# Optimization experiments

Hardware: AMD Instinct MI355X
Metric: run time of the kernel (lower is better)

The kernel has to match this reference:

```python
import jax, jax.numpy as jnp
import numpy as np
from jax import lax

B, V, K, E = 32768, 256, 4, 2048
INTERVENTION_STRENGTH = 1.0
PROP_SCALE = 0.1
N_ROUNDS = 3


def setup_inputs() -> dict:
    key = jax.random.key(0)
    ks = jax.random.split(key, 20)
    s = 0.02
    return {
        "original_data": jax.random.normal(ks[0], (B, V), jnp.float32),
        "intervention_values": jax.random.normal(ks[1], (B, K), jnp.float32),
        "strengths": jax.random.uniform(ks[2], (E,), jnp.float32),
        "intervention_variables": jnp.arange(K, dtype=jnp.int32),
        "cause_idx": jax.random.randint(ks[3], (E,), 0, V, jnp.int32),
        "effect_idx": jax.random.randint(ks[4], (E,), 0, V, jnp.int32),
        # per-intervention-variable estimator MLPs: Linear(V,64) -> ReLU -> Linear(64,V)
        "est_W1": jax.random.normal(ks[5], (K, 64, V), jnp.float32) * s,
        "est_b1": jnp.zeros((K, 64), jnp.float32),
        "est_W2": jax.random.normal(ks[6], (K, V, 64), jnp.float32) * s,
        "est_b2": jnp.zeros((K, V), jnp.float32),
        # plausibility scorer: Linear(3V,128) -> ReLU -> Linear(128,64) -> ReLU -> Linear(64,1) -> Sigmoid
        "pl_W1": jax.random.normal(ks[7], (128, 3 * V), jnp.float32) * s,
        "pl_b1": jnp.zeros((128,), jnp.float32),
        "pl_W2": jax.random.normal(ks[8], (64, 128), jnp.float32) * s,
        "pl_b2": jnp.zeros((64,), jnp.float32),
        "pl_W3": jax.random.normal(ks[9], (1, 64), jnp.float32) * s,
        "pl_b3": jnp.zeros((1,), jnp.float32),
    }


def _propagate(data, cause_idx, effect_idx, strengths):
    # Faithful sequential in-place edge updates (effect of edge k may feed edge k+1).
    def step(d, ces):
        c, e, st = ces
        infl = d[:, c] * (st * PROP_SCALE)  # [B]
        return d.at[:, e].add(infl), None

    def round_body(d, _):
        d, _ = lax.scan(step, d, (cause_idx, effect_idx, strengths))
        return d, None

    d, _ = lax.scan(round_body, data, None, length=N_ROUNDS)
    return d


def reference(original_data, intervention_values, strengths,
              est_W1, est_b1, est_W2, est_b2,
              pl_W1, pl_b1, pl_W2, pl_b2, pl_W3, pl_b3,
              intervention_variables, cause_idx, effect_idx):
    x = original_data  # [B, V]
    ivars = intervention_variables  # [K] int, constant

    # do-intervention: overwrite selected columns
    intervened = x.at[:, ivars].set(intervention_values)  # [B, V]

    # intervention effect estimators, vectorized over the K intervened variables
    h = jax.nn.relu(jnp.einsum('bv,kov->bko', x, est_W1) + est_b1)          # [B, K, 64]
    eff = jnp.einsum('bko,kvo->bkv', h, est_W2) + est_b2                     # [B, K, V]
    mag = jnp.abs(intervention_values - x[:, ivars])                         # [B, K]
    intervention_effects = jnp.einsum('bkv,bk->bv', eff, mag) * INTERVENTION_STRENGTH  # [B, V]

    # sequential causal propagation over edge list, 3 rounds
    final_cf = _propagate(intervened + intervention_effects, cause_idx, effect_idx, strengths)

    # plausibility scorer MLP
    pin = jnp.concatenate([x, intervened, final_cf], axis=1)                 # [B, 3V]
    p = jax.nn.relu(pin @ pl_W1.T + pl_b1)
    p = jax.nn.relu(p @ pl_W2.T + pl_b2)
    plaus = jax.nn.sigmoid(p @ pl_W3.T + pl_b3)                              # [B, 1]

    impact = jnp.linalg.norm(final_cf - x, axis=1, keepdims=True)            # [B, 1]
    return final_cf, intervention_effects, plaus, impact
```

## Files before the change

kernel.cpp:

```cpp
#include <hip/hip_runtime.h>

#define BDIM 32768
#define VDIM 256
#define KVAR 4
#define EDIM 2048
#define SEGS 16
#define SEGLEN 128

typedef __attribute__((ext_vector_type(8))) short short8;
typedef __attribute__((ext_vector_type(4))) float f32x4;

__device__ __forceinline__ unsigned short f2b(float f){
  union { float f; unsigned u; } v; v.f = f;
  unsigned r = v.u + 0x7FFFu + ((v.u >> 16) & 1u);
  return (unsigned short)(r >> 16);
}
__device__ __forceinline__ float b2f(unsigned short h){
  union { unsigned u; float f; } v; v.u = ((unsigned)h) << 16;
  return v.f;
}
__device__ __forceinline__ short8 ldb8(const unsigned short* p){
  return *(const short8*)p;
}

__device__ __forceinline__ void gl_lds16(const unsigned short* g, unsigned short* l){
  __builtin_amdgcn_global_load_lds(
      (const __attribute__((address_space(1))) unsigned int*)g,
      (__attribute__((address_space(3))) unsigned int*)l, 16, 0, 0);
}

__device__ __forceinline__ void stage256(const unsigned short* Bt, int kB,
                                         int w, int lane, unsigned short* Bs){
#pragma unroll
  for (int i = 0; i < 4; i++){
    int g8 = i*8 + w;
    int r  = g8*8 + (lane >> 3);
    int s  = lane & 7;
    gl_lds16(Bt + (size_t)r*VDIM + kB + ((s ^ (r & 7)) << 3),
             Bs + (size_t)g8*512);
  }
}
__device__ __forceinline__ void stage128(const unsigned short* Bt, int kB,
                                         int w, int lane, unsigned short* Bs){
#pragma unroll
  for (int i = 0; i < 2; i++){
    int g8 = i*8 + w;
    int r  = g8*8 + (lane >> 3);
    int s  = lane & 7;
    gl_lds16(Bt + (size_t)r*VDIM + kB + ((s ^ (r & 7)) << 3),
             Bs + (size_t)g8*512);
  }
}
__device__ __forceinline__ void stage64xb(const unsigned short* XBg, int rowBlk, int kB,
                                          int w, int lane, unsigned short* xbs){
  int r = w*8 + (lane >> 3);
  int s = lane & 7;
  gl_lds16(XBg + (size_t)(rowBlk + r)*VDIM + kB + ((s ^ (r & 7)) << 3),
           xbs + (size_t)w*512);
}

__device__ __forceinline__ short8 bs_frag(const unsigned short* Bs, int c, int klocal){
  int slot = klocal >> 3;
  return *(const short8*)&Bs[(size_t)c*64 + ((slot ^ (c & 7)) << 3)];
}

template<int NF>
__device__ __forceinline__ void mm_xA(const unsigned short* xbs, const unsigned short* Bs,
                                      int rl0, int c0, int kb, f32x4 (&acc)[2][NF])
{
  int sw = (rl0 & 7) << 3;
#pragma unroll
  for (int k = 0; k < 2; k++){
    int kl = k*32 + kb;
    short8 a0 = *(const short8*)&xbs[(size_t)rl0*64 + (kl ^ sw)];
    short8 a1 = *(const short8*)&xbs[(size_t)(rl0+16)*64 + (kl ^ sw)];
#pragma unroll
    for (int fn = 0; fn < NF; fn++){
      short8 b = bs_frag(Bs, c0 + fn*16, kl);
      acc[0][fn] = __builtin_amdgcn_mfma_f32_16x16x32_bf16(a0, b, acc[0][fn], 0, 0, 0);
      acc[1][fn] = __builtin_amdgcn_mfma_f32_16x16x32_bf16(a1, b, acc[1][fn], 0, 0, 0);
    }
  }
}
template<int NF>
__device__ __forceinline__ void mm_lA(const unsigned short* Alds, int ldaE,
                                      const unsigned short* Bs,
                                      int rl0, int c0, int kb, int kB,
                                      f32x4 (&acc)[2][NF])
{
  int sw = (rl0 & 7) << 3;
#pragma unroll
  for (int k = 0; k < 2; k++){
    int ka = kB + k*32 + kb;
    short8 a0 = *(const short8*)&Alds[(size_t)rl0 * ldaE + (ka ^ sw)];
    short8 a1 = *(const short8*)&Alds[(size_t)(rl0+16) * ldaE + (ka ^ sw)];
#pragma unroll
    for (int fn = 0; fn < NF; fn++){
      short8 b = bs_frag(Bs, c0 + fn*16, k*32 + kb);
      acc[0][fn] = __builtin_amdgcn_mfma_f32_16x16x32_bf16(a0, b, acc[0][fn], 0, 0, 0);
      acc[1][fn] = __builtin_amdgcn_mfma_f32_16x16x32_bf16(a1, b, acc[1][fn], 0, 0, 0);
    }
  }
}
template<int NF, int KSZ>
__device__ __forceinline__ void mm_l1(const unsigned short* Alds, int ldaE,
                                      const unsigned short* Bt, int ldb,
                                      int rl0, int c0, int kb,
                                      f32x4 (&acc)[NF])
{
  int sw = (rl0 & 7) << 3;
#pragma unroll
  for (int k0 = 0; k0 < KSZ; k0 += 32){
    int ka = k0 + kb;
    short8 a0 = *(const short8*)&Alds[(size_t)rl0 * ldaE + (ka ^ sw)];
#pragma unroll
    for (int fn = 0; fn < NF; fn++){
      short8 b = ldb8(Bt + (size_t)(c0 + fn*16)*ldb + ka);
      acc[fn] = __builtin_amdgcn_mfma_f32_16x16x32_bf16(a0, b, acc[fn], 0, 0, 0);
    }
  }
}

__global__ __launch_bounds__(256) void prep_seg(
    const float* X, const float* IV, const int* ivars,
    const float* eW1, const float* eW2, const float* pW1, const float* pW2,
    const int* cidx, const int* eidx, const float* stren,
    unsigned short* XB,
    unsigned short* bt1, unsigned short* bt2,
    unsigned short* w1ab, unsigned short* w1c,
    unsigned short* w2bf, float* w1bcol, int* colmap,
    float* delta, float* segs)
{
  if (blockIdx.x < 1024){
    __shared__ int lc[SEGLEN];
    __shared__ int le[SEGLEN];
    __shared__ float la[SEGLEN];
    int bid = blockIdx.x;
    int seg = bid >> 6;
    int rowbase = (bid & 63) * 4;
    int w = threadIdx.x >> 6, lane = threadIdx.x & 63;
    int row = rowbase + w;
    int k0 = seg * SEGLEN;
    for (int t = threadIdx.x; t < SEGLEN; t += 256){
      lc[t] = cidx[k0 + t]; le[t] = eidx[k0 + t]; la[t] = stren[k0 + t] * 0.1f;
    }
    __syncthreads();
    float r0 = (row == lane)        ? 1.f : 0.f;
    float r1 = (row == lane + 64)   ? 1.f : 0.f;
    float r2 = (row == lane + 128)  ? 1.f : 0.f;
    float r3 = (row == lane + 192)  ? 1.f : 0.f;
    for (int t = 0; t < SEGLEN; t++){
      int cs = __builtin_amdgcn_readfirstlane(lc[t]);
      int es = __builtin_amdgcn_readfirstlane(le[t]);
      float a = la[t];
      float vr;
      switch (cs >> 6){ case 0: vr = r0; break; case 1: vr = r1; break;
                        case 2: vr = r2; break; default: vr = r3; }
      float v = __shfl(vr, cs & 63, 64);
      float add = (lane == (es & 63)) ? a * v : 0.f;
      switch (es >> 6){ case 0: r0 += add; break; case 1: r1 += add; break;
                        case 2: r2 += add; break; default: r3 += add; }
    }
    float* out = segs + (size_t)seg * 65536 + (size_t)row * 256;
    out[lane] = r0; out[lane + 64] = r1; out[lane + 128] = r2; out[lane + 192] = r3;
    return;
  }
  int stride = 1024 * 256;
  int g0 = (blockIdx.x - 1024) * 256 + threadIdx.x;
  for (int i = g0; i < (BDIM * VDIM) / 8; i += stride){
    const float* p = X + (size_t)i * 8;
    f32x4 lo = *(const f32x4*)p;
    f32x4 hi = *(const f32x4*)(p + 4);
    short8 r;
    r[0]=(short)f2b(lo[0]); r[1]=(short)f2b(lo[1]); r[2]=(short)f2b(lo[2]); r[3]=(short)f2b(lo[3]);
    r[4]=(short)f2b(hi[0]); r[5]=(short)f2b(hi[1]); r[6]=(short)f2b(hi[2]); r[7]=(short)f2b(hi[3]);
    *(short8*)(XB + (size_t)i * 8) = r;
  }
  for (int i = g0; i < 65536; i += stride) bt1[i] = f2b(eW1[i]);
  for (int i = g0; i < 65536; i += stride){
    int v = i >> 8, r = i & 255;
    bt2[i] = f2b(eW2[(r >> 6) * 16384 + v * 64 + (r & 63)]);
  }
  for (int i = g0; i < 32768; i += stride){
    int o = i >> 8, v = i & 255;
    w1ab[i] = f2b(pW1[o*768 + v] + pW1[o*768 + 256 + v]);
    w1c[i]  = f2b(pW1[o*768 + 512 + v]);
  }
  for (int i = g0; i < 8192; i += stride) w2bf[i] = f2b(pW2[i]);
  for (int i = g0; i < 512; i += stride){
    int o = i >> 2, k = i & 3;
    w1bcol[i] = pW1[o*768 + 256 + ivars[k]];
  }
  for (int i = g0; i < VDIM; i += stride){
    int m = -1;
#pragma unroll
    for (int k = 0; k < KVAR; k++) if (ivars[k] == i) m = k;
    colmap[i] = m;
  }
  for (int i = g0; i < BDIM * KVAR; i += stride){
    int b = i >> 2, k = i & 3;
    delta[i] = IV[i] - X[(size_t)b * VDIM + ivars[k]];
  }
}

__global__ __launch_bounds__(256) void combine4(const float* S, float* Out)
{
  int m = blockIdx.x >> 6;
  int rb = (blockIdx.x & 63) * 4;
  int c = threadIdx.x;
  __shared__ float v[4][256];
  const float* base = S + (size_t)m * 4 * 65536;
#pragma unroll
  for (int r = 0; r < 4; r++) v[r][c] = base[(size_t)(rb + r) * 256 + c];
  __syncthreads();
  for (int p = 1; p < 4; p++){
    const float* Bm = base + (size_t)p * 65536;
    float a0 = 0.f, a1 = 0.f, a2 = 0.f, a3 = 0.f;
    for (int k = 0; k < 256; k += 4){
      f32x4 v0 = *(const f32x4*)&v[0][k];
      f32x4 v1 = *(const f32x4*)&v[1][k];
      f32x4 v2 = *(const f32x4*)&v[2][k];
      f32x4 v3 = *(const f32x4*)&v[3][k];
#pragma unroll
      for (int j = 0; j < 4; j++){
        float bk = Bm[(size_t)(k + j) * 256 + c];
        a0 += v0[j] * bk; a1 += v1[j] * bk; a2 += v2[j] * bk; a3 += v3[j] * bk;
      }
    }
    __syncthreads();
    v[0][c] = a0; v[1][c] = a1; v[2][c] = a2; v[3][c] = a3;
    __syncthreads();
  }
#pragma unroll
  for (int r = 0; r < 4; r++) Out[(size_t)m * 65536 + (size_t)(rb + r) * 256 + c] = v[r][c];
}

__global__ __launch_bounds__(256) void powM(const float* R, unsigned short* Mt)
{
  int rb = blockIdx.x * 4;
  int c = threadIdx.x;
  __shared__ float v[4][256];
#pragma unroll
  for (int r = 0; r < 4; r++) v[r][c] = R[(size_t)(rb + r) * 256 + c];
  __syncthreads();
  for (int p = 0; p < 2; p++){
    float a0 = 0.f, a1 = 0.f, a2 = 0.f, a3 = 0.f;
    for (int k = 0; k < 256; k += 4){
      f32x4 v0 = *(const f32x4*)&v[0][k];
      f32x4 v1 = *(const f32x4*)&v[1][k];
      f32x4 v2 = *(const f32x4*)&v[2][k];
      f32x4 v3 = *(const f32x4*)&v[3][k];
#pragma unroll
      for (int j = 0; j < 4; j++){
        float bk = R[(size_t)(k + j) * 256 + c];
        a0 += v0[j] * bk; a1 += v1[j] * bk; a2 += v2[j] * bk; a3 += v3[j] * bk;
      }
    }
    __syncthreads();
    v[0][c] = a0; v[1][c] = a1; v[2][c] = a2; v[3][c] = a3;
    __syncthreads();
  }
#pragma unroll
  for (int r = 0; r < 4; r++) Mt[(size_t)c * 256 + (rb + r)] = f2b(v[r][c]);
}

__global__ __launch_bounds__(512, 4) void mega(
    const float* IV, const unsigned short* XB,
    const unsigned short* Bt1, const unsigned short* Bt2, const unsigned short* Mt,
    const unsigned short* W1ab, const unsigned short* W1c, const unsigned short* W2bf,
    const float* eb1, const float* eb2, const float* delta, const int* colmap,
    const float* w1bcol, const float* pb1, const float* pb2,
    const float* W3, const float* pb3,
    float* effOut, float* outF, float* plausOut, float* impOut)
{
  __shared__ unsigned short buf[64 * 256];
  __shared__ unsigned short Bs[256 * 64];
  __shared__ unsigned short xbs[64 * 64];
  __shared__ float impLds[64 * 4];
  int tid = threadIdx.x, w = tid >> 6, lane = tid & 63;
  int rowg = w >> 2, colg = w & 3;
  int rowBlk = blockIdx.x * 64;
  int rl0 = rowg * 32 + (lane & 15);
  int colBase = colg * 64;
  int c0 = colBase + (lane & 15);
  int kb = (lane >> 4) * 8;
  f32x4 acc[2][4];
  unsigned short xcap[2][4][4];

#pragma unroll
  for (int fm = 0; fm < 2; fm++)
#pragma unroll
    for (int fn = 0; fn < 4; fn++) acc[fm][fn] = (f32x4){0.f,0.f,0.f,0.f};
  for (int kc = 0; kc < 4; kc++){
    int kB = kc * 64;
    stage256(Bt1, kB, w, lane, Bs);
    stage64xb(XB, rowBlk, kB, w, lane, xbs);
    __syncthreads();
    __builtin_amdgcn_s_setprio(1);
    mm_xA<4>(xbs, Bs, rl0, c0, kb, acc);
    __builtin_amdgcn_s_setprio(0);
    if (colg == kc){
#pragma unroll
      for (int fm = 0; fm < 2; fm++)
#pragma unroll
        for (int i = 0; i < 4; i++){
          int rl = rowg*32 + fm*16 + (lane >> 4)*4 + i;
          int sw = (rl & 7) << 3;
#pragma unroll
          for (int fn = 0; fn < 4; fn++){
            int lc = fn*16 + (lane & 15);
            xcap[fm][i][fn] = xbs[(size_t)rl*64 + (lc ^ sw)];
          }
        }
    }
    __syncthreads();
  }
  {
    float b1v[4];
#pragma unroll
    for (int fn = 0; fn < 4; fn++) b1v[fn] = eb1[colBase + fn*16 + (lane & 15)];
#pragma unroll
    for (int fm = 0; fm < 2; fm++)
#pragma unroll
      for (int i = 0; i < 4; i++){
        int rl = rowg*32 + fm*16 + (lane >> 4)*4 + i;
        int gr = rowBlk + rl;
        float mg = fabsf(delta[gr*4 + colg]);
        int sw = (rl & 7) << 3;
#pragma unroll
        for (int fn = 0; fn < 4; fn++){
          int col = colBase + fn*16 + (lane & 15);
          float h = acc[fm][fn][i] + b1v[fn];
          h = h > 0.f ? h : 0.f;
          buf[(size_t)rl*256 + (col ^ sw)] = f2b(h * mg);
        }
      }
  }
  __syncthreads();

#pragma unroll
  for (int fm = 0; fm < 2; fm++)
#pragma unroll
    for (int fn = 0; fn < 4; fn++) acc[fm][fn] = (f32x4){0.f,0.f,0.f,0.f};
  for (int kc = 0; kc < 4; kc++){
    int kB = kc * 64;
    stage256(Bt2, kB, w, lane, Bs);
    __syncthreads();
    __builtin_amdgcn_s_setprio(1);
    mm_lA<4>(buf, 256, Bs, rl0, c0, kb, kB, acc);
    __builtin_amdgcn_s_setprio(0);
    __syncthreads();
  }
  {
    float bb0[4], bb1[4], bb2[4], bb3[4];
    int imv[4];
#pragma unroll
    for (int fn = 0; fn < 4; fn++){
      int col = colBase + fn*16 + (lane & 15);
      bb0[fn] = eb2[col]; bb1[fn] = eb2[256 + col];
      bb2[fn] = eb2[512 + col]; bb3[fn] = eb2[768 + col];
      imv[fn] = colmap[col];
    }
#pragma unroll
    for (int fm = 0; fm < 2; fm++)
#pragma unroll
      for (int i = 0; i < 4; i++){
        int rl = rowg*32 + fm*16 + (lane >> 4)*4 + i;
        int gr = rowBlk + rl;
        f32x4 dl = *(const f32x4*)&delta[gr*4];
        float d0a = fabsf(dl[0]), d1a = fabsf(dl[1]), d2a = fabsf(dl[2]), d3a = fabsf(dl[3]);
        int sw = (rl & 7) << 3;
#pragma unroll
        for (int fn = 0; fn < 4; fn++){
          int col = colBase + fn*16 + (lane & 15);
          float eff = acc[fm][fn][i] + d0a*bb0[fn] + d1a*bb1[fn] + d2a*bb2[fn] + d3a*bb3[fn];
          size_t idx = (size_t)gr*VDIM + col;
          effOut[idx] = eff;
          float base = (imv[fn] >= 0) ? IV[gr*4 + imv[fn]] : b2f(xcap[fm][i][fn]);
          buf[(size_t)rl*256 + (col ^ sw)] = f2b(base + eff);
        }
      }
  }
  __syncthreads();

#pragma unroll
  for (int fm = 0; fm < 2; fm++)
#pragma unroll
    for (int fn = 0; fn < 4; fn++) acc[fm][fn] = (f32x4){0.f,0.f,0.f,0.f};
  for (int kc = 0; kc < 4; kc++){
    int kB = kc * 64;
    stage256(Mt, kB, w, lane, Bs);
    __syncthreads();
    __builtin_amdgcn_s_setprio(1);
    mm_lA<4>(buf, 256, Bs, rl0, c0, kb, kB, acc);
    __builtin_amdgcn_s_setprio(0);
    __syncthreads();
  }
  {
#pragma unroll
    for (int fm = 0; fm < 2; fm++)
#pragma unroll
      for (int i = 0; i < 4; i++){
        int rl = rowg*32 + fm*16 + (lane >> 4)*4 + i;
        int gr = rowBlk + rl;
        int sw = (rl & 7) << 3;
        float ss = 0.f;
#pragma unroll
        for (int fn = 0; fn < 4; fn++){
          int col = colBase + fn*16 + (lane & 15);
          size_t idx = (size_t)gr*VDIM + col;
          float fv = acc[fm][fn][i];
          outF[idx] = fv;
          buf[(size_t)rl*256 + (col ^ sw)] = f2b(fv);
          float d = fv - b2f(xcap[fm][i][fn]);
          ss += d * d;
        }
        ss += __shfl_xor(ss, 1, 64); ss += __shfl_xor(ss, 2, 64);
        ss += __shfl_xor(ss, 4, 64); ss += __shfl_xor(ss, 8, 64);
        if ((lane & 15) == 0) impLds[rl*4 + colg] = ss;
      }
  }
  __syncthreads();

  {
    f32x4 a4[2][2];
#pragma unroll
    for (int fm = 0; fm < 2; fm++)
#pragma unroll
      for (int fn = 0; fn < 2; fn++) a4[fm][fn] = (f32x4){0.f,0.f,0.f,0.f};
    int c4 = colg * 32 + (lane & 15);
    for (int kc = 0; kc < 4; kc++){
      int kB = kc * 64;
      stage128(W1ab, kB, w, lane, Bs);
      stage128(W1c,  kB, w, lane, Bs + 8192);
      stage64xb(XB, rowBlk, kB, w, lane, xbs);
      __syncthreads();
      __builtin_amdgcn_s_setprio(1);
      mm_xA<2>(xbs, Bs, rl0, c4, kb, a4);
      mm_lA<2>(buf, 256, Bs + 8192, rl0, c4, kb, kB, a4);
      __builtin_amdgcn_s_setprio(0);
      __syncthreads();
    }
    float bv[2];
    f32x4 wb[2];
#pragma unroll
    for (int fn = 0; fn < 2; fn++){
      int col = colg*32 + fn*16 + (lane & 15);
      bv[fn] = pb1[col];
      wb[fn] = *(const f32x4*)&w1bcol[col*4];
    }
#pragma unroll
    for (int fm = 0; fm < 2; fm++)
#pragma unroll
      for (int i = 0; i < 4; i++){
        int rl = rowg*32 + fm*16 + (lane >> 4)*4 + i;
        int gr = rowBlk + rl;
        f32x4 dl = *(const f32x4*)&delta[gr*4];
        int sw = (rl & 7) << 3;
#pragma unroll
        for (int fn = 0; fn < 2; fn++){
          int col = colg*32 + fn*16 + (lane & 15);
          float p = a4[fm][fn][i] + bv[fn]
                  + dl[0]*wb[fn][0] + dl[1]*wb[fn][1] + dl[2]*wb[fn][2] + dl[3]*wb[fn][3];
          p = p > 0.f ? p : 0.f;
          buf[(size_t)rl*128 + (col ^ sw)] = f2b(p);
        }
      }
  }
  __syncthreads();

  if (w < 4){
    int rl0b = w * 16 + (lane & 15);
    f32x4 a2[4];
#pragma unroll
    for (int fn = 0; fn < 4; fn++) a2[fn] = (f32x4){0.f,0.f,0.f,0.f};
    mm_l1<4, 128>(buf, 128, W2bf, 128, rl0b, (lane & 15), kb, a2);
    float b2v[4], w3v[4];
#pragma unroll
    for (int fn = 0; fn < 4; fn++){
      int col = fn*16 + (lane & 15);
      b2v[fn] = pb2[col]; w3v[fn] = W3[col];
    }
    float b3v = pb3[0];
#pragma unroll
    for (int i = 0; i < 4; i++){
      float s = 0.f;
#pragma unroll
      for (int fn = 0; fn < 4; fn++){
        float p2 = a2[fn][i] + b2v[fn];
        p2 = p2 > 0.f ? p2 : 0.f;
        s += p2 * w3v[fn];
      }
      s += __shfl_xor(s, 1, 64); s += __shfl_xor(s, 2, 64);
      s += __shfl_xor(s, 4, 64); s += __shfl_xor(s, 8, 64);
      if ((lane & 15) == 0){
        int gr = rowBlk + w*16 + (lane >> 4)*4 + i;
        plausOut[gr] = 1.f / (1.f + expf(-(s + b3v)));
      }
    }
  } else if (w == 4){
    f32x4 v = *(const f32x4*)&impLds[lane * 4];
    impOut[rowBlk + lane] = sqrtf(v[0] + v[1] + v[2] + v[3]);
  }
}

#define WS_XB     ((size_t)0)
#define WS_DELTA  ((size_t)16777216)
#define WS_SEG    ((size_t)17301504)
#define WS_T2     ((size_t)21495808)
#define WS_R      ((size_t)22544384)
#define WS_MT     ((size_t)22806528)
#define WS_BT1    ((size_t)22937600)
#define WS_BT2    ((size_t)23068672)
#define WS_W1AB   ((size_t)23199744)
#define WS_W1C    ((size_t)23265280)
#define WS_W2BF   ((size_t)23330816)
#define WS_W1BCOL ((size_t)23347200)
#define WS_COLMAP ((size_t)23349248)

extern "C" void kernel_launch(void* const* d_in, const int* in_sizes, int n_in,
                              void* d_out, int out_size, void* d_ws, size_t ws_size,
                              hipStream_t stream)
{
  const float* X     = (const float*)d_in[0];
  const float* IV    = (const float*)d_in[1];
  const float* STR   = (const float*)d_in[2];
  const int*   IVARS = (const int*)d_in[3];
  const int*   CIDX  = (const int*)d_in[4];
  const int*   EIDX  = (const int*)d_in[5];
  const float* EW1   = (const float*)d_in[6];
  const float* EB1   = (const float*)d_in[7];
  const float* EW2   = (const float*)d_in[8];
  const float* EB2   = (const float*)d_in[9];
  const float* PW1   = (const float*)d_in[10];
  const float* PB1   = (const float*)d_in[11];
  const float* PW2   = (const float*)d_in[12];
  const float* PB2   = (const float*)d_in[13];
  const float* PW3   = (const float*)d_in[14];
  const float* PB3   = (const float*)d_in[15];

  char* ws = (char*)d_ws;
  unsigned short* XB     = (unsigned short*)(ws + WS_XB);
  float*          DELTA  = (float*)(ws + WS_DELTA);
  float*          SEG    = (float*)(ws + WS_SEG);
  float*          T2     = (float*)(ws + WS_T2);
  float*          Rm     = (float*)(ws + WS_R);
  unsigned short* MT     = (unsigned short*)(ws + WS_MT);
  unsigned short* BT1    = (unsigned short*)(ws + WS_BT1);
  unsigned short* BT2    = (unsigned short*)(ws + WS_BT2);
  unsigned short* W1AB   = (unsigned short*)(ws + WS_W1AB);
  unsigned short* W1C    = (unsigned short*)(ws + WS_W1C);
  unsigned short* W2BF   = (unsigned short*)(ws + WS_W2BF);
  float*          W1BCOL = (float*)(ws + WS_W1BCOL);
  int*            COLMAP = (int*)(ws + WS_COLMAP);

  float* outF   = (float*)d_out;
  float* outEff = outF + (size_t)BDIM * VDIM;
  float* outPl  = outEff + (size_t)BDIM * VDIM;
  float* outIm  = outPl + BDIM;

  prep_seg<<<2048, 256, 0, stream>>>(X, IV, IVARS, EW1, EW2, PW1, PW2,
                                     CIDX, EIDX, STR,
                                     XB, BT1, BT2, W1AB, W1C, W2BF, W1BCOL, COLMAP,
                                     DELTA, SEG);
  combine4<<<256, 256, 0, stream>>>(SEG, T2);
  combine4<<<64, 256, 0, stream>>>(T2, Rm);
  powM<<<64, 256, 0, stream>>>(Rm, MT);

  mega<<<512, 512, 0, stream>>>(IV, XB, BT1, BT2, MT, W1AB, W1C, W2BF,
                                EB1, EB2, DELTA, COLMAP, W1BCOL,
                                PB1, PB2, PW3, PB3,
                                outEff, outF, outPl, outIm);

  (void)in_sizes; (void)n_in; (void)out_size; (void)ws_size;
}
```

Before: 193.5 us.

## Split fused mega kernel into five streaming GEMM kernels via workspace

```diff
diff --git a/kernel.cpp b/kernel.cpp
--- a/kernel.cpp
+++ b/kernel.cpp
@@ -29,6 +29,43 @@
       (__attribute__((address_space(3))) unsigned int*)l, 16, 0, 0);
 }
 
+template<int NF, int KSZ>
+__device__ __forceinline__ void mm_g2(const unsigned short* A, int lda,
+                                      const unsigned short* Bt, int ldb,
+                                      int r0, int c0, int kb,
+                                      f32x4 (&acc)[2][NF])
+{
+#pragma unroll
+  for (int k0 = 0; k0 < KSZ; k0 += 32){
+    int ka = k0 + kb;
+    short8 a0 = ldb8(A + (size_t)r0*lda + ka);
+    short8 a1 = ldb8(A + (size_t)(r0+16)*lda + ka);
+#pragma unroll
+    for (int fn = 0; fn < NF; fn++){
+      short8 b = ldb8(Bt + (size_t)(c0 + fn*16)*ldb + ka);
+      acc[0][fn] = __builtin_amdgcn_mfma_f32_16x16x32_bf16(a0, b, acc[0][fn], 0, 0, 0);
+      acc[1][fn] = __builtin_amdgcn_mfma_f32_16x16x32_bf16(a1, b, acc[1][fn], 0, 0, 0);
+    }
+  }
+}
+template<int NF, int KSZ>
+__device__ __forceinline__ void mm_g1(const unsigned short* A, int lda,
+                                      const unsigned short* Bt, int ldb,
+                                      int r0, int c0, int kb,
+                                      f32x4 (&acc)[NF])
+{
+#pragma unroll
+  for (int k0 = 0; k0 < KSZ; k0 += 32){
+    int ka = k0 + kb;
+    short8 a0 = ldb8(A + (size_t)r0*lda + ka);
+#pragma unroll
+    for (int fn = 0; fn < NF; fn++){
+      short8 b = ldb8(Bt + (size_t)(c0 + fn*16)*ldb + ka);
+      acc[fn] = __builtin_amdgcn_mfma_f32_16x16x32_bf16(a0, b, acc[fn], 0, 0, 0);
+    }
+  }
+}
+
 __device__ __forceinline__ void stage256(const unsigned short* Bt, int kB,
                                          int w, int lane, unsigned short* Bs){
 #pragma unroll
@@ -58,12 +95,10 @@
   gl_lds16(XBg + (size_t)(rowBlk + r)*VDIM + kB + ((s ^ (r & 7)) << 3),
            xbs + (size_t)w*512);
 }
-
 __device__ __forceinline__ short8 bs_frag(const unsigned short* Bs, int c, int klocal){
   int slot = klocal >> 3;
   return *(const short8*)&Bs[(size_t)c*64 + ((slot ^ (c & 7)) << 3)];
 }
-
 template<int NF>
 __device__ __forceinline__ void mm_xA(const unsigned short* xbs, const unsigned short* Bs,
                                       int rl0, int c0, int kb, f32x4 (&acc)[2][NF])
@@ -264,6 +299,212 @@
   for (int r = 0; r < 4; r++) Mt[(size_t)c * 256 + (rb + r)] = f2b(v[r][c]);
 }
 
+
+__global__ __launch_bounds__(256) void gemmH(
+    const unsigned short* XB, const unsigned short* Bt1,
+    const float* eb1, const float* delta, unsigned short* Hs)
+{
+  int tid = threadIdx.x, w = tid >> 6, lane = tid & 63;
+  int rowBlk = blockIdx.x * 32;
+  int r0 = rowBlk + (lane & 15);
+  int colBase = w * 64;
+  int c0 = colBase + (lane & 15);
+  int kb = (lane >> 4) * 8;
+  f32x4 acc[2][4];
+#pragma unroll
+  for (int fm = 0; fm < 2; fm++)
+#pragma unroll
+    for (int fn = 0; fn < 4; fn++) acc[fm][fn] = (f32x4){0.f,0.f,0.f,0.f};
+  mm_g2<4, VDIM>(XB, VDIM, Bt1, VDIM, r0, c0, kb, acc);
+  float b1v[4];
+#pragma unroll
+  for (int fn = 0; fn < 4; fn++) b1v[fn] = eb1[colBase + fn*16 + (lane & 15)];
+#pragma unroll
+  for (int fm = 0; fm < 2; fm++)
+#pragma unroll
+    for (int i = 0; i < 4; i++){
+      int gr = rowBlk + fm*16 + (lane >> 4)*4 + i;
+      float mg = fabsf(delta[gr*4 + w]);
+#pragma unroll
+      for (int fn = 0; fn < 4; fn++){
+        int col = colBase + fn*16 + (lane & 15);
+        float h = acc[fm][fn][i] + b1v[fn];
+        h = h > 0.f ? h : 0.f;
+        Hs[(size_t)gr*VDIM + col] = f2b(h * mg);
+      }
+    }
+}
+
+__global__ __launch_bounds__(256) void gemmEff(
+    const unsigned short* Hs, const unsigned short* Bt2, const unsigned short* XB,
+    const float* eb2, const float* delta, const int* colmap, const float* IV,
+    float* effOut, unsigned short* DB)
+{
+  int tid = threadIdx.x, w = tid >> 6, lane = tid & 63;
+  int rowBlk = blockIdx.x * 32;
+  int r0 = rowBlk + (lane & 15);
+  int colBase = w * 64;
+  int c0 = colBase + (lane & 15);
+  int kb = (lane >> 4) * 8;
+  f32x4 acc[2][4];
+#pragma unroll
+  for (int fm = 0; fm < 2; fm++)
+#pragma unroll
+    for (int fn = 0; fn < 4; fn++) acc[fm][fn] = (f32x4){0.f,0.f,0.f,0.f};
+  mm_g2<4, VDIM>(Hs, VDIM, Bt2, VDIM, r0, c0, kb, acc);
+  float bb0[4], bb1[4], bb2[4], bb3[4];
+  int imv[4];
+#pragma unroll
+  for (int fn = 0; fn < 4; fn++){
+    int col = colBase + fn*16 + (lane & 15);
+    bb0[fn] = eb2[col]; bb1[fn] = eb2[256 + col];
+    bb2[fn] = eb2[512 + col]; bb3[fn] = eb2[768 + col];
+    imv[fn] = colmap[col];
+  }
+#pragma unroll
+  for (int fm = 0; fm < 2; fm++)
+#pragma unroll
+    for (int i = 0; i < 4; i++){
+      int gr = rowBlk + fm*16 + (lane >> 4)*4 + i;
+      f32x4 dl = *(const f32x4*)&delta[gr*4];
+      float d0a = fabsf(dl[0]), d1a = fabsf(dl[1]), d2a = fabsf(dl[2]), d3a = fabsf(dl[3]);
+#pragma unroll
+      for (int fn = 0; fn < 4; fn++){
+        int col = colBase + fn*16 + (lane & 15);
+        float eff = acc[fm][fn][i] + d0a*bb0[fn] + d1a*bb1[fn] + d2a*bb2[fn] + d3a*bb3[fn];
+        size_t idx = (size_t)gr*VDIM + col;
+        effOut[idx] = eff;
+        float base = (imv[fn] >= 0) ? IV[gr*4 + imv[fn]] : b2f(XB[idx]);
+        DB[idx] = f2b(base + eff);
+      }
+    }
+}
+
+__global__ __launch_bounds__(256) void gemmFin(
+    const unsigned short* DB, const unsigned short* Mt, const unsigned short* XB,
+    float* outF, unsigned short* FinB, float* impOut)
+{
+  __shared__ float impLds[32 * 4];
+  int tid = threadIdx.x, w = tid >> 6, lane = tid & 63;
+  int rowBlk = blockIdx.x * 32;
+  int r0 = rowBlk + (lane & 15);
+  int colBase = w * 64;
+  int c0 = colBase + (lane & 15);
+  int kb = (lane >> 4) * 8;
+  f32x4 acc[2][4];
+#pragma unroll
+  for (int fm = 0; fm < 2; fm++)
+#pragma unroll
+    for (int fn = 0; fn < 4; fn++) acc[fm][fn] = (f32x4){0.f,0.f,0.f,0.f};
+  mm_g2<4, VDIM>(DB, VDIM, Mt, VDIM, r0, c0, kb, acc);
+#pragma unroll
+  for (int fm = 0; fm < 2; fm++)
+#pragma unroll
+    for (int i = 0; i < 4; i++){
+      int rl = fm*16 + (lane >> 4)*4 + i;
+      int gr = rowBlk + rl;
+      float ss = 0.f;
+#pragma unroll
+      for (int fn = 0; fn < 4; fn++){
+        int col = colBase + fn*16 + (lane & 15);
+        size_t idx = (size_t)gr*VDIM + col;
+        float fv = acc[fm][fn][i];
+        outF[idx] = fv;
+        FinB[idx] = f2b(fv);
+        float d = fv - b2f(XB[idx]);
+        ss += d * d;
+      }
+      ss += __shfl_xor(ss, 1, 64); ss += __shfl_xor(ss, 2, 64);
+      ss += __shfl_xor(ss, 4, 64); ss += __shfl_xor(ss, 8, 64);
+      if ((lane & 15) == 0) impLds[rl*4 + w] = ss;
+    }
+  __syncthreads();
+  if (tid < 32){
+    f32x4 v = *(const f32x4*)&impLds[tid * 4];
+    impOut[rowBlk + tid] = sqrtf(v[0] + v[1] + v[2] + v[3]);
+  }
+}
+
+__global__ __launch_bounds__(256) void gemmP1(
+    const unsigned short* XB, const unsigned short* FinB,
+    const unsigned short* W1ab, const unsigned short* W1c,
+    const float* pb1, const float* w1bcol, const float* delta,
+    unsigned short* P1B)
+{
+  int tid = threadIdx.x, w = tid >> 6, lane = tid & 63;
+  int rowBlk = blockIdx.x * 32;
+  int r0 = rowBlk + (lane & 15);
+  int c4 = w*32 + (lane & 15);
+  int kb = (lane >> 4) * 8;
+  f32x4 a4[2][2];
+#pragma unroll
+  for (int fm = 0; fm < 2; fm++)
+#pragma unroll
+    for (int fn = 0; fn < 2; fn++) a4[fm][fn] = (f32x4){0.f,0.f,0.f,0.f};
+  mm_g2<2, VDIM>(XB, VDIM, W1ab, VDIM, r0, c4, kb, a4);
+  mm_g2<2, VDIM>(FinB, VDIM, W1c, VDIM, r0, c4, kb, a4);
+  float bv[2];
+  f32x4 wb[2];
+#pragma unroll
+  for (int fn = 0; fn < 2; fn++){
+    int col = w*32 + fn*16 + (lane & 15);
+    bv[fn] = pb1[col];
+    wb[fn] = *(const f32x4*)&w1bcol[col*4];
+  }
+#pragma unroll
+  for (int fm = 0; fm < 2; fm++)
+#pragma unroll
+    for (int i = 0; i < 4; i++){
+      int gr = rowBlk + fm*16 + (lane >> 4)*4 + i;
+      f32x4 dl = *(const f32x4*)&delta[gr*4];
+#pragma unroll
+      for (int fn = 0; fn < 2; fn++){
+        int col = w*32 + fn*16 + (lane & 15);
+        float p = a4[fm][fn][i] + bv[fn]
+                + dl[0]*wb[fn][0] + dl[1]*wb[fn][1] + dl[2]*wb[fn][2] + dl[3]*wb[fn][3];
+        p = p > 0.f ? p : 0.f;
+        P1B[(size_t)gr*128 + col] = f2b(p);
+      }
+    }
+}
+
+__global__ __launch_bounds__(256) void gemmP2(
+    const unsigned short* P1B, const unsigned short* W2bf,
+    const float* pb2, const float* W3, const float* pb3, float* plausOut)
+{
+  int tid = threadIdx.x, w = tid >> 6, lane = tid & 63;
+  int rowBlk = blockIdx.x * 64;
+  int r0b = rowBlk + w*16 + (lane & 15);
+  int kb = (lane >> 4) * 8;
+  f32x4 a2[4];
+#pragma unroll
+  for (int fn = 0; fn < 4; fn++) a2[fn] = (f32x4){0.f,0.f,0.f,0.f};
+  mm_g1<4, 128>(P1B, 128, W2bf, 128, r0b, (lane & 15), kb, a2);
+  float b2v[4], w3v[4];
+#pragma unroll
+  for (int fn = 0; fn < 4; fn++){
+    int col = fn*16 + (lane & 15);
+    b2v[fn] = pb2[col]; w3v[fn] = W3[col];
+  }
+  float b3v = pb3[0];
+#pragma unroll
+  for (int i = 0; i < 4; i++){
+    float s = 0.f;
+#pragma unroll
+    for (int fn = 0; fn < 4; fn++){
+      float p2 = a2[fn][i] + b2v[fn];
+      p2 = p2 > 0.f ? p2 : 0.f;
+      s += p2 * w3v[fn];
+    }
+    s += __shfl_xor(s, 1, 64); s += __shfl_xor(s, 2, 64);
+    s += __shfl_xor(s, 4, 64); s += __shfl_xor(s, 8, 64);
+    if ((lane & 15) == 0){
+      int gr = rowBlk + w*16 + (lane >> 4)*4 + i;
+      plausOut[gr] = 1.f / (1.f + expf(-(s + b3v)));
+    }
+  }
+}
+
 __global__ __launch_bounds__(512, 4) void mega(
     const float* IV, const unsigned short* XB,
     const unsigned short* Bt1, const unsigned short* Bt2, const unsigned short* Mt,
@@ -517,6 +758,9 @@
 #define WS_W2BF   ((size_t)23330816)
 #define WS_W1BCOL ((size_t)23347200)
 #define WS_COLMAP ((size_t)23349248)
+#define WS_HS     ((size_t)25165824)
+#define WS_DB     ((size_t)41943040)
+#define WS_NEED   ((size_t)58720256)
 
 extern "C" void kernel_launch(void* const* d_in, const int* in_sizes, int n_in,
                               void* d_out, int out_size, void* d_ws, size_t ws_size,
@@ -553,6 +797,10 @@
   unsigned short* W2BF   = (unsigned short*)(ws + WS_W2BF);
   float*          W1BCOL = (float*)(ws + WS_W1BCOL);
   int*            COLMAP = (int*)(ws + WS_COLMAP);
+  unsigned short* HS     = (unsigned short*)(ws + WS_HS);
+  unsigned short* DB     = (unsigned short*)(ws + WS_DB);
+  unsigned short* FINB   = HS;
+  unsigned short* P1B    = DB;
 
   float* outF   = (float*)d_out;
   float* outEff = outF + (size_t)BDIM * VDIM;
@@ -567,10 +815,20 @@
   combine4<<<64, 256, 0, stream>>>(T2, Rm);
   powM<<<64, 256, 0, stream>>>(Rm, MT);
 
-  mega<<<512, 512, 0, stream>>>(IV, XB, BT1, BT2, MT, W1AB, W1C, W2BF,
-                                EB1, EB2, DELTA, COLMAP, W1BCOL,
-                                PB1, PB2, PW3, PB3,
-                                outEff, outF, outPl, outIm);
-
-  (void)in_sizes; (void)n_in; (void)out_size; (void)ws_size;
-}
+  if (ws_size >= WS_NEED){
+    gemmH  <<<1024, 256, 0, stream>>>(XB, BT1, EB1, DELTA, HS);
+    gemmEff<<<1024, 256, 0, stream>>>(HS, BT2, XB, EB2, DELTA, COLMAP, IV,
+                                      outEff, DB);
+    gemmFin<<<1024, 256, 0, stream>>>(DB, MT, XB, outF, FINB, outIm);
+    gemmP1 <<<1024, 256, 0, stream>>>(XB, FINB, W1AB, W1C, PB1, W1BCOL, DELTA,
+                                      P1B);
+    gemmP2 <<<512, 256, 0, stream>>>(P1B, W2BF, PB2, PW3, PB3, outPl);
+  } else {
+    mega<<<512, 512, 0, stream>>>(IV, XB, BT1, BT2, MT, W1AB, W1C, W2BF,
+                                  EB1, EB2, DELTA, COLMAP, W1BCOL,
+                                  PB1, PB2, PW3, PB3,
+                                  outEff, outF, outPl, outIm);
+  }
+
+  (void)in_sizes; (void)n_in; (void)out_size;
+}
```

Measured after the change: 254.6 us. +31.6%, slower.
